# Kernel optimization log

Measured on AMD Instinct MI355X. Metric: run time of the kernel, lower is better.

Reference implementation:

```python
import jax, jax.numpy as jnp
import numpy as np
from jax import lax

# dims
B, N, K = 8, 1024, 32          # batch, nodes, kNN neighbors
D, H, DH = 256, 8, 32           # node feature width, heads, head dim
TDIM, NB, HID = 16, 32, 128     # time-embed dim, radial basis count, radial MLP hidden
NLAYERS = 3                     # hidden transformer layers
L = NLAYERS + 1                 # + output layer
NS = 128                        # scalar channels sliced into edge attrs
SHD = 9                         # spherical harmonics dim for lmax=2 (1+3+5)
RMAX = 2.0
EIN = NB + TDIM + 2 * NS        # edge-MLP input width


def _sph(u):
    # real spherical harmonics l=0,1,2 with 'component' normalization of unit vec u
    x, y, z = u[..., 0], u[..., 1], u[..., 2]
    l0 = jnp.ones_like(x)[..., None]
    l1 = np.sqrt(3.0) * u
    l2 = jnp.stack([
        np.sqrt(15.0) * x * y,
        np.sqrt(15.0) * y * z,
        0.5 * np.sqrt(5.0) * (3.0 * z * z - 1.0),
        np.sqrt(15.0) * x * z,
        0.5 * np.sqrt(15.0) * (x * x - y * y),
    ], -1)
    return jnp.concatenate([l0, l1, l2], -1)


def _rbf(r):
    # e3nn soft_one_hot_linspace(basis='gaussian', cutoff=False) * sqrt(NB) * 0.95
    centers = jnp.linspace(0.0, RMAX, NB)
    step = RMAX / (NB - 1)
    e = jnp.exp(-((r[..., None] - centers) / step) ** 2) / 1.12
    return e * (NB ** 0.5) * 0.95


def _sus(x):
    # e3nn smooth unit step: exp(-1/x) for x>0 else 0
    return jnp.where(x > 0, jnp.exp(-1.0 / jnp.where(x > 0, x, 1.0)), 0.0)


def setup_inputs() -> dict:
    key = jax.random.key(0)
    ks = jax.random.split(key, 12)
    g = lambda k, shape, fan: (jax.random.normal(k, shape, jnp.float32) / np.sqrt(fan))
    return {
        'x': jax.random.normal(ks[0], (B, N, 3), jnp.float32),
        'y': jax.random.normal(ks[1], (B, N, 3), jnp.float32),
        't': jax.random.uniform(ks[2], (B, TDIM), jnp.float32),
        'W_embed': g(ks[3], (3 + TDIM, D), 3 + TDIM),
        'Wk1': g(ks[4], (L, EIN, HID), EIN),
        'bk1': jnp.zeros((L, HID), jnp.float32),
        'Wk2': g(ks[5], (L, HID, H * DH), HID),
        'Wq': g(ks[6], (L, D, H * DH), D),
        'Wv': g(ks[7], (L, D + SHD, H * DH), D + SHD),
        'Wo': g(ks[8], (NLAYERS, H * DH, D), H * DH),
        'Wo_out': g(ks[9], (H * DH, 3), H * DH),
    }


def _forward(x, y, t, W_embed, Wk1, bk1, Wk2, Wq, Wv, Wo, Wo_out):
    def score(pos, feat, tt):
        # kNN graph: full pairwise distance + top_k (self included, as in source)
        d2 = jnp.sum((pos[:, None, :] - pos[None, :, :]) ** 2, -1)      # [N,N]
        src = lax.top_k(-d2, K)[1]                                       # [N,K], dst = row index
        vec = pos[:, None, :] - pos[src]                                 # pos[dst]-pos[src], [N,K,3]
        r = jnp.linalg.norm(vec, axis=-1)                                # [N,K]
        u = vec / jnp.maximum(r[..., None], 1e-9)
        sh = _sph(u)                                                     # [N,K,SHD]
        cut = 1.4 * _sus(10.0 * (1.0 - r / RMAX))                        # [N,K]
        rbf = _rbf(r) * cut[..., None]                                   # [N,K,NB]
        t_nodes = jnp.broadcast_to(tt, (N, TDIM))
        edge_base = jnp.concatenate([rbf, jnp.broadcast_to(tt, (N, K, TDIM))], -1)
        node = jnp.concatenate([feat, t_nodes], -1) @ W_embed            # [N,D]
        for l in range(L):
            # gather scalar node channels onto edges
            e = jnp.concatenate([edge_base, node[src][..., :NS],
                                 jnp.broadcast_to(node[:, None, :NS], (N, K, NS))], -1)  # [N,K,EIN]
            h = jax.nn.gelu(e @ Wk1[l] + bk1[l])                          # radial MLP
            kf = (h @ Wk2[l]).reshape(N, K, H, DH)
            q = (node @ Wq[l]).reshape(N, H, DH)
            logits = jnp.einsum('nhd,nkhd->nkh', q, kf) / np.sqrt(DH)
            # cutoff-weighted softmax over neighbors (e3nn Transformer style)
            w = cut[..., None] * jnp.exp(logits - logits.max(1, keepdims=True))
            alpha = w / (w.sum(1, keepdims=True) + 1e-9)                  # [N,K,H]
            v = (jnp.concatenate([node[src], sh], -1) @ Wv[l]).reshape(N, K, H, DH)
            agg = jnp.einsum('nkh,nkhd->nhd', alpha, v).reshape(N, H * DH)
            if l < NLAYERS:
                node = node + agg @ Wo[l]                                  # residual
                # scalar activation: gelu on 0e, tanh on 0o, identity on higher l
                node = jnp.concatenate([jax.nn.gelu(node[:, :64]),
                                        jnp.tanh(node[:, 64:NS]),
                                        node[:, NS:]], -1)
            else:
                node = agg @ Wo_out                                        # project to 1x1e
        return node  # [N,3]

    return jax.vmap(score)(x, y, t)


def reference(x, y, t, W_embed, Wk1, bk1, Wk2, Wq, Wv, Wo, Wo_out):
    return _forward(x, y, t, W_embed, Wk1, bk1, Wk2, Wq, Wv, Wo, Wo_out)
```

## Files before the change

### kernel.cpp

```cpp
#include <hip/hip_runtime.h>
#include <math.h>

#define Bb 8
#define Nn 1024
#define Kk 32
#define Dd 256
#define Hh 8
#define DHh 32
#define TDIMt 16
#define NBnb 32
#define HIDh 128
#define NSns 128
#define SHDs 9
#define EINe 304
#define NCOLS 1536

typedef __bf16 bf16_t;
typedef bf16_t bf16x8 __attribute__((ext_vector_type(8)));
typedef float floatx4 __attribute__((ext_vector_type(4)));

#define GLOAD_LDS16(gp, lp) __builtin_amdgcn_global_load_lds( \
    (const __attribute__((address_space(1))) void*)(gp),      \
    (__attribute__((address_space(3))) void*)(lp), 16, 0, 0)

__device__ __forceinline__ float gelu_fast(float x){
  float g = 1.5957691216057308f*(x + 0.044715f*x*x*x);
  return x*__builtin_amdgcn_rcpf(1.0f + __expf(-g));
}
__device__ __forceinline__ float tanh_fast(float x){
  return 1.0f - 2.0f*__builtin_amdgcn_rcpf(1.0f + __expf(2.0f*x));
}

__global__ __launch_bounds__(256) void setup_kernel(
    const float* __restrict__ x, const float* __restrict__ y, const float* __restrict__ t,
    const float* __restrict__ We, const float* __restrict__ Wk1, const float* __restrict__ bk1,
    const float* __restrict__ Wk2, const float* __restrict__ Wq, const float* __restrict__ Wv,
    const float* __restrict__ Wo,
    bf16_t* __restrict__ Wt, bf16_t* __restrict__ Wto, bf16_t* __restrict__ WrbfT,
    float* __restrict__ t_hd, int* __restrict__ src,
    float* __restrict__ node, bf16_t* __restrict__ node_bf){

  __shared__ float s_b[32];
  __shared__ unsigned long long s_knn[4][64];
  const int bid = blockIdx.x, tid = threadIdx.x;

  if (bid < 2048){
    int wave = tid >> 6, lane = tid & 63;
    int bn = bid*4 + wave;
    int b = bn >> 10, n = bn & (Nn-1);
    const float* xb = x + (size_t)b*Nn*3;
    float px = xb[n*3+0], py = xb[n*3+1], pz = xb[n*3+2];
    float d2v[16];
    #pragma unroll
    for (int i=0;i<16;i++){
      int j = i*64 + lane;
      float dx = px - xb[j*3+0];
      float dy = py - xb[j*3+1];
      float dz = pz - xb[j*3+2];
      d2v[i] = dx*dx + dy*dy + dz*dz;
    }

    unsigned lob = 0u, hib = 0x7149F2CAu;
    float T = 1.0f;
    int lc = 0;
    for (int it=0; it<24; ++it){
      lc = 0;
      #pragma unroll
      for (int i=0;i<16;i++) lc += (d2v[i] <= T) ? 1 : 0;
      int c = lc;
      #pragma unroll
      for (int off=32; off>=1; off>>=1) c += __shfl_xor(c, off);
      if (c >= 32 && c <= 64) break;
      if (c < 32) lob = __float_as_uint(T); else hib = __float_as_uint(T);
      float ratio = 44.0f * __builtin_amdgcn_rcpf((float)(c < 1 ? 1 : c));
      float Tn = T * __powf(ratio, 0.6666667f);
      unsigned tb = __float_as_uint(Tn);
      if (tb <= lob || tb >= hib) tb = lob + ((hib - lob) >> 1);
      T = __uint_as_float(tb);
    }

    int pre = lc;
    #pragma unroll
    for (int d=1; d<64; d<<=1){
      int o = __shfl_up(pre, d);
      if (lane >= d) pre += o;
    }
    int wo = pre - lc;

    unsigned long long* sl = s_knn[wave];
    sl[lane] = ~0ull;
    #pragma unroll
    for (int i=0;i<16;i++){
      if (d2v[i] <= T && wo < 64){
        sl[wo] = (((unsigned long long)__float_as_uint(d2v[i])) << 10)
                 | (unsigned)(i*64 + lane);
        wo++;
      }
    }
    __syncthreads();

    unsigned long long key = sl[lane];
    #pragma unroll
    for (int k2=2; k2<=64; k2<<=1){
      #pragma unroll
      for (int j2=k2>>1; j2>=1; j2>>=1){
        unsigned long long pv = __shfl_xor(key, j2);
        bool takeMin = (((lane & j2) == 0) == ((lane & k2) == 0));
        bool pLess = pv < key;
        key = (pLess == takeMin) ? pv : key;
      }
    }
    if (lane < 32) src[(size_t)bn*Kk + lane] = (int)(key & 1023u);
  } else if (bid < 6144){
    int i = bid-2048; int l = i>>10, yy = i&1023;
    int h = yy>>7, c = yy&127;
    if (tid < 32) s_b[tid] = Wk2[(size_t)l*HIDh*Dd + (size_t)c*Dd + h*DHh + tid];
    __syncthreads();
    const int rloc = tid>>3, dg = tid&7;
    const float b0 = s_b[dg*4+0], b1 = s_b[dg*4+1], b2 = s_b[dg*4+2], b3 = s_b[dg*4+3];
    #pragma unroll
    for (int p=0;p<8;p++){
      int ii = p*32 + rloc;
      const float4 v = *(const float4*)(Wq + (size_t)l*Dd*Dd + (size_t)ii*Dd + h*DHh + dg*4);
      float part = v.x*b0 + v.y*b1 + v.z*b2 + v.w*b3;
      part += __shfl_xor(part, 1);
      part += __shfl_xor(part, 2);
      part += __shfl_xor(part, 4);
      if (dg == 0) Wt[((size_t)l*NCOLS + 512 + yy)*Dd + ii] = (bf16_t)part;
    }
  } else if (bid < 8192){
    int i = bid-6144; int l = i>>9, c = i&511, k = tid;
    const float* wk1l = Wk1 + (size_t)l*EINe*HIDh;
    float v;
    if (c < 256)       v = Wv[(size_t)l*265*Dd + (size_t)k*Dd + c];
    else if (c < 384){ int c2 = c-256; v = (k < 128) ? wk1l[(48+k)*HIDh + c2] : 0.0f; }
    else             { int c2 = c-384; v = (k < 128) ? wk1l[(176+k)*HIDh + c2] : 0.0f; }
    Wt[((size_t)l*NCOLS + c)*Dd + k] = (bf16_t)v;
  } else if (bid < 8960){
    int i = bid-8192; int l = i>>8; int c = i&255; int k = tid;
    Wto[((size_t)l*Dd + c)*Dd + k] = (bf16_t)Wo[(size_t)l*Dd*Dd + (size_t)k*Dd + c];
  } else if (bid < 9024){
    int i = bid-8960; int l = i>>4, cg = i&15;
    int c = cg*8 + (tid>>5), k = tid&31;
    WrbfT[((size_t)l*HIDh + c)*NBnb + k] = (bf16_t)Wk1[(size_t)l*EINe*HIDh + (size_t)k*HIDh + c];
  } else if (bid < 9040){
    int i = bid-9024; int pair = i*2 + (tid>>7);
    int l = pair>>3, b = pair&7, c = tid&127;
    const float* wk1l = Wk1 + (size_t)l*EINe*HIDh;
    float a = bk1[l*HIDh + c];
    #pragma unroll
    for (int ii=0;ii<TDIMt;ii++) a += t[b*TDIMt+ii]*wk1l[(32+ii)*HIDh + c];
    t_hd[(l*Bb + b)*HIDh + c] = a;
  } else {
    int bn0 = (bid-9040)*4; int c = tid;
    float w0 = We[0*Dd+c], w1 = We[1*Dd+c], w2 = We[2*Dd+c];
    float wt[TDIMt];
    #pragma unroll
    for (int i=0;i<TDIMt;i++) wt[i] = We[(3+i)*Dd+c];
    #pragma unroll
    for (int u=0;u<4;u++){
      int bn = bn0 + u; int b = bn >> 10;
      float a = y[(size_t)bn*3+0]*w0 + y[(size_t)bn*3+1]*w1 + y[(size_t)bn*3+2]*w2;
      #pragma unroll
      for (int i=0;i<TDIMt;i++) a += t[b*TDIMt+i]*wt[i];
      node[(size_t)bn*Dd + c] = a;
      node_bf[(size_t)bn*Dd + c] = (bf16_t)a;
    }
  }
}

__global__ __launch_bounds__(256) void gemm_proj(const bf16_t* __restrict__ A,
    const bf16_t* __restrict__ Wt_all, float* __restrict__ vproj_f,
    bf16_t* __restrict__ hsrc_bf, float* __restrict__ hdst_f,
    bf16_t* __restrict__ qw_bf, const float* __restrict__ t_hd, int layer){

  __shared__ __align__(16) bf16_t s_A[2][8192];
  __shared__ __align__(16) bf16_t s_B[2][4096];

  const int tid = threadIdx.x;
  const int wave = tid>>6, lane = tid&63;
  const int row16 = lane&15, quad = lane>>4;
  const int bx = blockIdx.x;
  const int brow = ((bx & 7) << 3) + (bx >> 3);
  const int m0 = brow*128;
  const int m_base = m0 + wave*32;
  const int n_base = blockIdx.y*64;
  const bf16_t* Ab = A + (size_t)m0*Dd;
  const bf16_t* Bw = Wt_all + ((size_t)layer*NCOLS + n_base)*Dd;

  const int trow = tid>>3;
  const int tk   = ((tid&7) ^ (trow&7)) << 3;
  const int swz  = (row16&7) << 3;

  floatx4 acc[2][4];
  #pragma unroll
  for (int mi=0;mi<2;mi++)
    #pragma unroll
    for (int ni=0;ni<4;ni++){ floatx4 z = {0.f,0.f,0.f,0.f}; acc[mi][ni] = z; }

  {
    const bf16_t* ga = Ab + (size_t)trow*Dd + tk;
    #pragma unroll
    for (int i=0;i<4;i++) GLOAD_LDS16(ga + (size_t)i*32*Dd, &s_A[0][i*2048 + tid*8]);
    const bf16_t* gb = Bw + (size_t)trow*Dd + tk;
    #pragma unroll
    for (int j=0;j<2;j++) GLOAD_LDS16(gb + (size_t)j*32*Dd, &s_B[0][j*2048 + tid*8]);
  }
  __syncthreads();

  #pragma unroll
  for (int kt=0; kt<4; kt++){
    const int cur = kt&1, nxt = cur^1;
    if (kt < 3){
      const bf16_t* ga = Ab + (size_t)trow*Dd + (kt+1)*64 + tk;
      #pragma unroll
      for (int i=0;i<4;i++) GLOAD_LDS16(ga + (size_t)i*32*Dd, &s_A[nxt][i*2048 + tid*8]);
      const bf16_t* gb = Bw + (size_t)trow*Dd + (kt+1)*64 + tk;
      #pragma unroll
      for (int j=0;j<2;j++) GLOAD_LDS16(gb + (size_t)j*32*Dd, &s_B[nxt][j*2048 + tid*8]);
    }
    #pragma unroll
    for (int ksub=0; ksub<2; ksub++){
      const int ko = (ksub*32 + quad*8) ^ swz;
      bf16x8 a0 = *(const bf16x8*)&s_A[cur][(wave*32      + row16)*64 + ko];
      bf16x8 a1 = *(const bf16x8*)&s_A[cur][(wave*32 + 16 + row16)*64 + ko];
      #pragma unroll
      for (int ni=0;ni<4;ni++){
        bf16x8 b = *(const bf16x8*)&s_B[cur][(ni*16 + row16)*64 + ko];
        acc[0][ni] = __builtin_amdgcn_mfma_f32_16x16x32_bf16(a0, b, acc[0][ni], 0,0,0);
        acc[1][ni] = __builtin_amdgcn_mfma_f32_16x16x32_bf16(a1, b, acc[1][ni], 0,0,0);
      }
    }
    __syncthreads();
  }

  const int by = blockIdx.y;
  const int bb = m_base >> 10;
  #pragma unroll
  for (int mi=0;mi<2;mi++)
    #pragma unroll
    for (int ni=0;ni<4;ni++){
      int col = n_base + ni*16 + row16;
      #pragma unroll
      for (int r=0;r<4;r++){
        int row = m_base + mi*16 + quad*4 + r;
        float v = acc[mi][ni][r];
        if (by < 4)       vproj_f[(size_t)row*256 + col]        = v;
        else if (by < 6)  hsrc_bf[(size_t)row*128 + (col-256)]  = (bf16_t)v;
        else if (by < 8)  hdst_f[(size_t)row*128 + (col-384)]   = v + t_hd[(size_t)(layer*Bb + bb)*HIDh + (col-384)];
        else              qw_bf[(size_t)row*1024 + (col-512)]   = (bf16_t)v;
      }
    }
}

__global__ __launch_bounds__(256) void gemm_upd(
    const bf16_t* __restrict__ agg_bf, const bf16_t* __restrict__ Wto,
    const float* __restrict__ node_in, float* __restrict__ node_out,
    bf16_t* __restrict__ node_bf, int lu, int write_node){

  __shared__ __align__(16) bf16_t s_A[2][8192];
  __shared__ __align__(16) bf16_t s_B[2][4096];

  const int tid = threadIdx.x;
  const int wave = tid>>6, lane = tid&63;
  const int row16 = lane&15, quad = lane>>4;
  const int bx = blockIdx.x;
  const int brow = ((bx & 7) << 3) + (bx >> 3);
  const int m0 = brow*128;
  const int m_base = m0 + wave*32;
  const int n_base = blockIdx.y*64;
  const bf16_t* Ab = agg_bf + (size_t)m0*Dd;
  const bf16_t* Bw = Wto + (size_t)lu*Dd*Dd + (size_t)n_base*Dd;

  const int trow = tid>>3;
  const int tk   = ((tid&7) ^ (trow&7)) << 3;
  const int swz  = (row16&7) << 3;

  floatx4 acc[2][4];
  #pragma unroll
  for (int mi=0;mi<2;mi++)
    #pragma unroll
    for (int ni=0;ni<4;ni++){ floatx4 z = {0.f,0.f,0.f,0.f}; acc[mi][ni] = z; }

  {
    const bf16_t* ga = Ab + (size_t)trow*Dd + tk;
    #pragma unroll
    for (int i=0;i<4;i++) GLOAD_LDS16(ga + (size_t)i*32*Dd, &s_A[0][i*2048 + tid*8]);
    const bf16_t* gb = Bw + (size_t)trow*Dd + tk;
    #pragma unroll
    for (int j=0;j<2;j++) GLOAD_LDS16(gb + (size_t)j*32*Dd, &s_B[0][j*2048 + tid*8]);
  }
  __syncthreads();

  #pragma unroll
  for (int kt=0; kt<4; kt++){
    const int cur = kt&1, nxt = cur^1;
    if (kt < 3){
      const bf16_t* ga = Ab + (size_t)trow*Dd + (kt+1)*64 + tk;
      #pragma unroll
      for (int i=0;i<4;i++) GLOAD_LDS16(ga + (size_t)i*32*Dd, &s_A[nxt][i*2048 + tid*8]);
      const bf16_t* gb = Bw + (size_t)trow*Dd + (kt+1)*64 + tk;
      #pragma unroll
      for (int j=0;j<2;j++) GLOAD_LDS16(gb + (size_t)j*32*Dd, &s_B[nxt][j*2048 + tid*8]);
    }
    #pragma unroll
    for (int ksub=0; ksub<2; ksub++){
      const int ko = (ksub*32 + quad*8) ^ swz;
      bf16x8 a0 = *(const bf16x8*)&s_A[cur][(wave*32      + row16)*64 + ko];
      bf16x8 a1 = *(const bf16x8*)&s_A[cur][(wave*32 + 16 + row16)*64 + ko];
      #pragma unroll
      for (int ni=0;ni<4;ni++){
        bf16x8 b = *(const bf16x8*)&s_B[cur][(ni*16 + row16)*64 + ko];
        acc[0][ni] = __builtin_amdgcn_mfma_f32_16x16x32_bf16(a0, b, acc[0][ni], 0,0,0);
        acc[1][ni] = __builtin_amdgcn_mfma_f32_16x16x32_bf16(a1, b, acc[1][ni], 0,0,0);
      }
    }
    __syncthreads();
  }

  #pragma unroll
  for (int mi=0;mi<2;mi++)
    #pragma unroll
    for (int ni=0;ni<4;ni++){
      int col = n_base + ni*16 + row16;
      #pragma unroll
      for (int r=0;r<4;r++){
        int row = m_base + mi*16 + quad*4 + r;
        float v = acc[mi][ni][r] + node_in[(size_t)row*Dd + col];
        if (col < 64)       v = gelu_fast(v);
        else if (col < 128) v = tanh_fast(v);
        if (write_node) node_out[(size_t)row*Dd + col] = v;
        node_bf[(size_t)row*Dd + col] = (bf16_t)v;
      }
    }
}

__global__ __launch_bounds__(256) void attn_kernel(
    const float* __restrict__ x, const int* __restrict__ src,
    const float* __restrict__ vproj_f, const bf16_t* __restrict__ hsrc_bf,
    const float* __restrict__ hdst_f, const bf16_t* __restrict__ qw_bf,
    const bf16_t* __restrict__ WrbfT,
    const float* __restrict__ Wvg, const float* __restrict__ Woo,
    bf16_t* __restrict__ agg_bf, float* __restrict__ out, int layer){

  __shared__ __align__(16) char smem[11632];
  bf16_t* s_h     = (bf16_t*)(smem);
  float*  s_part  = (float*)(smem);
  float*  s_sh    = (float*)(smem + 8704);
  float*  s_cut   = (float*)(smem + 9984);
  int*    s_srcv  = (int*)  (smem + 10112);
  float*  s_logit = (float*)(smem + 10240);
  float*  s_poolsh= (float*)(smem + 11264);
  float*  s_red   = (float*)(smem + 11584);

  const int tid = threadIdx.x;
  const int bidx = blockIdx.x;
  const int bn  = ((bidx & 7) << 10) | (bidx >> 3);
  const int b   = bn >> 10;
  const int wave = tid>>6, lane = tid&63;
  const int row16 = lane&15, quad = lane>>4;

  bf16x8 qf[4];
  if (wave < 2){
    const bf16_t* qp = qw_bf + (size_t)bn*1024 + row16*HIDh + quad*8;
    #pragma unroll
    for (int ks=0; ks<4; ks++) qf[ks] = *(const bf16x8*)(qp + ks*32);
  }
  const float hdv0 = hdst_f[(size_t)bn*128 + wave*32 + row16];
  const float hdv1 = hdst_f[(size_t)bn*128 + wave*32 + 16 + row16];

  const float ax = x[(size_t)bn*3+0], ay = x[(size_t)bn*3+1], az = x[(size_t)bn*3+2];

  const int hr = tid>>4;
  const int hc = tid&15;
  const int sH0 = src[(size_t)bn*Kk + hr];
  const int sH1 = src[(size_t)bn*Kk + hr + 16];
  const int sE0 = src[(size_t)bn*Kk + row16];
  const int sE1 = src[(size_t)bn*Kk + row16 + 16];
  bf16x8 hsv0 = *(const bf16x8*)(hsrc_bf + ((size_t)b*Nn + sH0)*128 + hc*8);
  bf16x8 hsv1 = *(const bf16x8*)(hsrc_bf + ((size_t)b*Nn + sH1)*128 + hc*8);

  bf16x8 a0f, a1f;
  {
    const float* xj0 = x + ((size_t)b*Nn + sE0)*3;
    const float* xj1 = x + ((size_t)b*Nn + sE1)*3;
    float d0x = ax - xj0[0], d0y = ay - xj0[1], d0z = az - xj0[2];
    float d1x = ax - xj1[0], d1y = ay - xj1[1], d1z = az - xj1[2];
    float rr0 = sqrtf(d0x*d0x + d0y*d0y + d0z*d0z);
    float rr1 = sqrtf(d1x*d1x + d1y*d1y + d1z*d1z);
    float xx0 = 10.0f*(1.0f - rr0*0.5f);
    float xx1 = 10.0f*(1.0f - rr1*0.5f);
    float cu0 = (xx0 > 0.0f) ? 1.4f*__expf(-__builtin_amdgcn_rcpf(xx0)) : 0.0f;
    float cu1 = (xx1 > 0.0f) ? 1.4f*__expf(-__builtin_amdgcn_rcpf(xx1)) : 0.0f;
    float sc0 = 4.798224586623f*cu0;
    float sc1 = 4.798224586623f*cu1;
    float rs0 = fminf(rr0*15.5f, 33.0f);
    float rs1 = fminf(rr1*15.5f, 33.0f);
    float cbase = (float)(quad*8);
    float dd0 = rs0 - cbase, dd1 = rs1 - cbase;
    float e0 = __expf(-dd0*dd0)*sc0;
    float e1 = __expf(-dd1*dd1)*sc1;
    float g0 = __expf(2.0f*dd0 - 1.0f);
    float g1 = __expf(2.0f*dd1 - 1.0f);
    a0f[0] = (bf16_t)e0; a1f[0] = (bf16_t)e1;
    #pragma unroll
    for (int j=1;j<8;j++){
      e0 *= g0; e1 *= g1;
      a0f[j] = (bf16_t)e0; a1f[j] = (bf16_t)e1;
      g0 *= 0.13533528323661270f; g1 *= 0.13533528323661270f;
    }
  }

  if (tid < 32){
    int k = tid;
    int j = src[(size_t)bn*Kk + k];
    s_srcv[k] = j;
    const float* xj = x + ((size_t)b*Nn + j)*3;
    float dx = ax - xj[0], dy = ay - xj[1], dz = az - xj[2];
    float rr = sqrtf(dx*dx + dy*dy + dz*dz);
    float xx = 10.0f*(1.0f - rr*0.5f);
    s_cut[k] = (xx > 0.0f) ? 1.4f*__expf(-__builtin_amdgcn_rcpf(xx)) : 0.0f;
  } else if (tid < 64){
    int k = tid - 32;
    int j = src[(size_t)bn*Kk + k];
    const float* xj = x + ((size_t)b*Nn + j)*3;
    float dx = ax - xj[0], dy = ay - xj[1], dz = az - xj[2];
    float rr = sqrtf(dx*dx + dy*dy + dz*dz);
    float inv = __builtin_amdgcn_rcpf(fmaxf(rr, 1e-9f));
    float ux = dx*inv, uy = dy*inv, uz = dz*inv;
    float* sh = s_sh + k*10;
    sh[0] = 1.0f;
    sh[1] = 1.7320508075688772f*ux;
    sh[2] = 1.7320508075688772f*uy;
    sh[3] = 1.7320508075688772f*uz;
    sh[4] = 3.872983346207417f*ux*uy;
    sh[5] = 3.872983346207417f*uy*uz;
    sh[6] = 1.118033988749895f*(3.0f*uz*uz - 1.0f);
    sh[7] = 3.872983346207417f*ux*uz;
    sh[8] = 1.9364916731037085f*(ux*ux - uy*uy);
  }

  floatx4 acc[2][2];
  {
    #pragma unroll
    for (int mi=0;mi<2;mi++)
      #pragma unroll
      for (int ni=0;ni<2;ni++){ floatx4 z = {0.f,0.f,0.f,0.f}; acc[mi][ni] = z; }
    const bf16_t* bp = WrbfT + ((size_t)layer*HIDh + wave*32 + row16)*NBnb + quad*8;
    bf16x8 b0 = *(const bf16x8*)(bp);
    bf16x8 b1 = *(const bf16x8*)(bp + 16*NBnb);
    acc[0][0] = __builtin_amdgcn_mfma_f32_16x16x32_bf16(a0f, b0, acc[0][0], 0,0,0);
    acc[0][1] = __builtin_amdgcn_mfma_f32_16x16x32_bf16(a0f, b1, acc[0][1], 0,0,0);
    acc[1][0] = __builtin_amdgcn_mfma_f32_16x16x32_bf16(a1f, b0, acc[1][0], 0,0,0);
    acc[1][1] = __builtin_amdgcn_mfma_f32_16x16x32_bf16(a1f, b1, acc[1][1], 0,0,0);
  }
  *(bf16x8*)(s_h + hr*136 + hc*8)      = hsv0;
  *(bf16x8*)(s_h + (hr+16)*136 + hc*8) = hsv1;
  __syncthreads();

  #pragma unroll
  for (int ni=0;ni<2;ni++){
    int c = wave*32 + ni*16 + row16;
    float hdv = ni ? hdv1 : hdv0;
    #pragma unroll
    for (int mi=0;mi<2;mi++){
      #pragma unroll
      for (int r=0;r<4;r++){
        int e = mi*16 + quad*4 + r;
        float hs = (float)s_h[e*136 + c];
        s_h[e*136 + c] = (bf16_t)gelu_fast(acc[mi][ni][r] + hdv + hs);
      }
    }
  }
  __syncthreads();

  if (wave < 2){
    floatx4 la = {0.f,0.f,0.f,0.f};
    #pragma unroll
    for (int ks=0; ks<4; ks++){
      bf16x8 a = *(const bf16x8*)(s_h + (wave*16 + row16)*136 + ks*32 + quad*8);
      la = __builtin_amdgcn_mfma_f32_16x16x32_bf16(a, qf[ks], la, 0,0,0);
    }
    if (row16 < Hh){
      #pragma unroll
      for (int r=0;r<4;r++)
        s_logit[(wave*16 + quad*4 + r)*8 + row16] = la[r]*0.17677669529663687f;
    }
  }
  __syncthreads();

  {
    const int k = tid & 31;
    const int h = tid >> 5;
    float lv = s_logit[k*8 + h];
    float m = lv;
    #pragma unroll
    for (int off=16; off>=1; off>>=1) m = fmaxf(m, __shfl_xor(m, off));
    float w = s_cut[k]*__expf(lv - m);
    float ss = w;
    #pragma unroll
    for (int off=16; off>=1; off>>=1) ss += __shfl_xor(ss, off);
    float alpha = w*__builtin_amdgcn_rcpf(ss + 1e-9f);
    s_logit[k*8 + h] = alpha;
  }
  __syncthreads();

  {
    const float* rowp[8];
    #pragma unroll
    for (int i=0;i<8;i++){
      int row = __builtin_amdgcn_readfirstlane(s_srcv[wave*8 + i]);
      rowp[i] = vproj_f + ((size_t)b*Nn + row)*256;
    }
    const int al_base = wave*64 + (lane>>3);
    float4 accv = {0.f,0.f,0.f,0.f};
    #pragma unroll
    for (int i=0;i<8;i++){
      const float4 v = *(const float4*)(rowp[i] + (lane<<2));
      float al = s_logit[al_base + i*8];
      accv.x += al*v.x; accv.y += al*v.y; accv.z += al*v.z; accv.w += al*v.w;
    }

    if (wave >= 2){
      const int tt = tid - 128;
      const int h2 = tt >> 4, sg = tt & 15;
      if (sg < SHDs){
        float a = 0.0f;
        #pragma unroll
        for (int k2=0;k2<Kk;k2++)
          a += s_logit[k2*8 + h2] * s_sh[k2*10 + sg];
        s_poolsh[h2*10 + sg] = a;
      }
    }

    *(float4*)(s_part + wave*256 + (lane<<2)) = accv;
  }
  __syncthreads();

  {
    const int h = tid >> 5;
    float a_main = s_part[tid] + s_part[256+tid] + s_part[512+tid] + s_part[768+tid];

    const float* wvsh = Wvg + (size_t)layer*265*Dd + 256*Dd;
    #pragma unroll
    for (int sg=0; sg<SHDs; sg++) a_main += s_poolsh[h*10 + sg]*wvsh[sg*Dd + tid];

    if (layer < 3){
      agg_bf[(size_t)bn*Dd + tid] = (bf16_t)a_main;
    } else {
      float p0 = a_main*Woo[tid*3+0];
      float p1 = a_main*Woo[tid*3+1];
      float p2 = a_main*Woo[tid*3+2];
      #pragma unroll
      for (int off=32; off>=1; off>>=1){
        p0 += __shfl_xor(p0, off);
        p1 += __shfl_xor(p1, off);
        p2 += __shfl_xor(p2, off);
      }
      if (lane == 0){ s_red[wave*3+0]=p0; s_red[wave*3+1]=p1; s_red[wave*3+2]=p2; }
      __syncthreads();
      if (tid < 3)
        out[(size_t)bn*3 + tid] = s_red[0*3+tid]+s_red[1*3+tid]+s_red[2*3+tid]+s_red[3*3+tid];
    }
  }
}

extern "C" void kernel_launch(void* const* d_in, const int* in_sizes, int n_in,
                              void* d_out, int out_size, void* d_ws, size_t ws_size,
                              hipStream_t stream){
  const float* x   = (const float*)d_in[0];
  const float* y   = (const float*)d_in[1];
  const float* t   = (const float*)d_in[2];
  const float* We  = (const float*)d_in[3];
  const float* Wk1 = (const float*)d_in[4];
  const float* bk1 = (const float*)d_in[5];
  const float* Wk2 = (const float*)d_in[6];
  const float* Wq  = (const float*)d_in[7];
  const float* Wv  = (const float*)d_in[8];
  const float* Wo  = (const float*)d_in[9];
  const float* Woo = (const float*)d_in[10];
  float* out = (float*)d_out;

  char* ws = (char*)d_ws;
  size_t off = 0;
  auto take = [&](size_t bytes)->char*{ char* p = ws + off; off = (off + bytes + 255) & ~(size_t)255; return p; };

  int*    src      = (int*)   take((size_t)Bb*Nn*Kk*4);
  float*  nodeA    = (float*) take((size_t)Bb*Nn*Dd*4);
  float*  nodeB    = (float*) take((size_t)Bb*Nn*Dd*4);
  bf16_t* node_bf  = (bf16_t*)take((size_t)Bb*Nn*Dd*2);
  bf16_t* agg_bf   = (bf16_t*)take((size_t)Bb*Nn*Dd*2);
  float*  vproj_f  = (float*) take((size_t)Bb*Nn*256*4);
  bf16_t* hsrc_bf  = (bf16_t*)take((size_t)Bb*Nn*128*2);
  float*  hdst_f   = (float*) take((size_t)Bb*Nn*128*4);
  bf16_t* qw_bf    = (bf16_t*)take(((size_t)Bb*Nn*1024 + 2048)*2);
  bf16_t* Wt       = (bf16_t*)take((size_t)4*NCOLS*Dd*2);
  bf16_t* Wto      = (bf16_t*)take((size_t)3*Dd*Dd*2);
  bf16_t* WrbfT    = (bf16_t*)take((size_t)4*HIDh*NBnb*2);
  float*  t_hd     = (float*) take((size_t)4*Bb*HIDh*4);

  setup_kernel<<<dim3(11088), 256, 0, stream>>>(x, y, t, We, Wk1, bk1, Wk2, Wq, Wv, Wo,
                                                Wt, Wto, WrbfT, t_hd, src, nodeA, node_bf);

  gemm_proj<<<dim3(64,24), 256, 0, stream>>>(node_bf, Wt, vproj_f, hsrc_bf, hdst_f, qw_bf, t_hd, 0);
  attn_kernel<<<dim3(Bb*Nn), 256, 0, stream>>>(x, src, vproj_f, hsrc_bf, hdst_f, qw_bf,
                                               WrbfT, Wv, Woo, agg_bf, out, 0);
  const float* nin[3]  = {nodeA, nodeB, nodeA};
  float*       nout[3] = {nodeB, nodeA, nodeB};
  for (int l=1; l<4; l++){
    gemm_upd<<<dim3(64,4), 256, 0, stream>>>(agg_bf, Wto, nin[l-1], nout[l-1], node_bf,
                                             l-1, (l < 3) ? 1 : 0);
    gemm_proj<<<dim3(64,24), 256, 0, stream>>>(node_bf, Wt, vproj_f, hsrc_bf, hdst_f, qw_bf, t_hd, l);
    attn_kernel<<<dim3(Bb*Nn), 256, 0, stream>>>(x, src, vproj_f, hsrc_bf, hdst_f, qw_bf,
                                                 WrbfT, Wv, Woo, agg_bf, out, l);
  }
}
```

Baseline: 404.9 us.

## Process two destination nodes per attention block to use all waves

The attention kernel now handles two nodes per 256-thread block, with two waves per node, and the grid is halved. Before, only two of the four waves did the logit MFMA and the other waves idled or did side work. Now every wave does MFMA work, and the Wv spherical-harmonic weights and RBF weight loads are shared across two nodes. Shared memory roughly doubles, and each wave handles 16 neighbor rows of value gathers, so per-wave latency and register pressure rise and occupancy may drop.

```diff
diff --git a/kernel.cpp b/kernel.cpp
--- a/kernel.cpp
+++ b/kernel.cpp
@@ -343,42 +343,46 @@
     const float* __restrict__ Wvg, const float* __restrict__ Woo,
     bf16_t* __restrict__ agg_bf, float* __restrict__ out, int layer){
 
-  __shared__ __align__(16) char smem[11632];
+  __shared__ __align__(16) char smem[23296];
   bf16_t* s_h     = (bf16_t*)(smem);
   float*  s_part  = (float*)(smem);
-  float*  s_sh    = (float*)(smem + 8704);
-  float*  s_cut   = (float*)(smem + 9984);
-  int*    s_srcv  = (int*)  (smem + 10112);
-  float*  s_logit = (float*)(smem + 10240);
-  float*  s_poolsh= (float*)(smem + 11264);
-  float*  s_red   = (float*)(smem + 11584);
-
-  const int tid = threadIdx.x;
+  float*  s_sh    = (float*)(smem + 17408);
+  float*  s_cut   = (float*)(smem + 19968);
+  int*    s_srcv  = (int*)  (smem + 20224);
+  float*  s_logit = (float*)(smem + 20480);
+  float*  s_pool  = (float*)(smem + 22528);
+  float*  s_red   = (float*)(smem + 23168);
+
+  const int tid  = threadIdx.x;
   const int bidx = blockIdx.x;
-  const int bn  = ((bidx & 7) << 10) | (bidx >> 3);
-  const int b   = bn >> 10;
+  const int b    = bidx & 7;
+  const int bn0  = (b << 10) | ((bidx >> 3) << 1);
   const int wave = tid>>6, lane = tid&63;
+  const int side = wave>>1, wv = wave&1;
   const int row16 = lane&15, quad = lane>>4;
+  const int bns = bn0 + side;
 
   bf16x8 qf[4];
-  if (wave < 2){
-    const bf16_t* qp = qw_bf + (size_t)bn*1024 + row16*HIDh + quad*8;
-    #pragma unroll
-    for (int ks=0; ks<4; ks++) qf[ks] = *(const bf16x8*)(qp + ks*32);
-  }
-  const float hdv0 = hdst_f[(size_t)bn*128 + wave*32 + row16];
-  const float hdv1 = hdst_f[(size_t)bn*128 + wave*32 + 16 + row16];
-
-  const float ax = x[(size_t)bn*3+0], ay = x[(size_t)bn*3+1], az = x[(size_t)bn*3+2];
-
-  const int hr = tid>>4;
-  const int hc = tid&15;
-  const int sH0 = src[(size_t)bn*Kk + hr];
-  const int sH1 = src[(size_t)bn*Kk + hr + 16];
-  const int sE0 = src[(size_t)bn*Kk + row16];
-  const int sE1 = src[(size_t)bn*Kk + row16 + 16];
-  bf16x8 hsv0 = *(const bf16x8*)(hsrc_bf + ((size_t)b*Nn + sH0)*128 + hc*8);
-  bf16x8 hsv1 = *(const bf16x8*)(hsrc_bf + ((size_t)b*Nn + sH1)*128 + hc*8);
+  { const bf16_t* qp = qw_bf + (size_t)bns*1024 + row16*HIDh + quad*8;
+    #pragma unroll
+    for (int ks=0; ks<4; ks++) qf[ks] = *(const bf16x8*)(qp + ks*32); }
+  float hdv[4];
+  #pragma unroll
+  for (int ni=0; ni<4; ni++) hdv[ni] = hdst_f[(size_t)bns*128 + wv*64 + ni*16 + row16];
+
+  const float ax = x[(size_t)bns*3+0], ay = x[(size_t)bns*3+1], az = x[(size_t)bns*3+2];
+
+  const int sE0 = src[(size_t)bns*Kk + row16];
+  const int sE1 = src[(size_t)bns*Kk + row16 + 16];
+
+  const int t2 = tid & 127;
+  const int e0 = t2>>3, cg = t2&7;
+  const int sG0 = src[(size_t)bns*Kk + e0];
+  const int sG1 = src[(size_t)bns*Kk + e0 + 16];
+  bf16x8 hsv00 = *(const bf16x8*)(hsrc_bf + ((size_t)b*Nn + sG0)*128 + cg*8);
+  bf16x8 hsv01 = *(const bf16x8*)(hsrc_bf + ((size_t)b*Nn + sG0)*128 + cg*8 + 64);
+  bf16x8 hsv10 = *(const bf16x8*)(hsrc_bf + ((size_t)b*Nn + sG1)*128 + cg*8);
+  bf16x8 hsv11 = *(const bf16x8*)(hsrc_bf + ((size_t)b*Nn + sG1)*128 + cg*8 + 64);
 
   bf16x8 a0f, a1f;
   {
@@ -398,93 +402,96 @@
     float rs1 = fminf(rr1*15.5f, 33.0f);
     float cbase = (float)(quad*8);
     float dd0 = rs0 - cbase, dd1 = rs1 - cbase;
-    float e0 = __expf(-dd0*dd0)*sc0;
-    float e1 = __expf(-dd1*dd1)*sc1;
+    float e0v = __expf(-dd0*dd0)*sc0;
+    float e1v = __expf(-dd1*dd1)*sc1;
     float g0 = __expf(2.0f*dd0 - 1.0f);
     float g1 = __expf(2.0f*dd1 - 1.0f);
-    a0f[0] = (bf16_t)e0; a1f[0] = (bf16_t)e1;
+    a0f[0] = (bf16_t)e0v; a1f[0] = (bf16_t)e1v;
     #pragma unroll
     for (int j=1;j<8;j++){
-      e0 *= g0; e1 *= g1;
-      a0f[j] = (bf16_t)e0; a1f[j] = (bf16_t)e1;
+      e0v *= g0; e1v *= g1;
+      a0f[j] = (bf16_t)e0v; a1f[j] = (bf16_t)e1v;
       g0 *= 0.13533528323661270f; g1 *= 0.13533528323661270f;
     }
   }
 
-  if (tid < 32){
-    int k = tid;
-    int j = src[(size_t)bn*Kk + k];
-    s_srcv[k] = j;
+  if (tid < 128){
+    const int hs = (tid>>6)&1;
+    const int k = tid & 31;
+    const int hn = bn0 + hs;
+    const int j = src[(size_t)hn*Kk + k];
+    const float hx = x[(size_t)hn*3+0], hy = x[(size_t)hn*3+1], hz = x[(size_t)hn*3+2];
     const float* xj = x + ((size_t)b*Nn + j)*3;
-    float dx = ax - xj[0], dy = ay - xj[1], dz = az - xj[2];
+    float dx = hx - xj[0], dy = hy - xj[1], dz = hz - xj[2];
     float rr = sqrtf(dx*dx + dy*dy + dz*dz);
-    float xx = 10.0f*(1.0f - rr*0.5f);
-    s_cut[k] = (xx > 0.0f) ? 1.4f*__expf(-__builtin_amdgcn_rcpf(xx)) : 0.0f;
-  } else if (tid < 64){
-    int k = tid - 32;
-    int j = src[(size_t)bn*Kk + k];
-    const float* xj = x + ((size_t)b*Nn + j)*3;
-    float dx = ax - xj[0], dy = ay - xj[1], dz = az - xj[2];
-    float rr = sqrtf(dx*dx + dy*dy + dz*dz);
-    float inv = __builtin_amdgcn_rcpf(fmaxf(rr, 1e-9f));
-    float ux = dx*inv, uy = dy*inv, uz = dz*inv;
-    float* sh = s_sh + k*10;
-    sh[0] = 1.0f;
-    sh[1] = 1.7320508075688772f*ux;
-    sh[2] = 1.7320508075688772f*uy;
-    sh[3] = 1.7320508075688772f*uz;
-    sh[4] = 3.872983346207417f*ux*uy;
-    sh[5] = 3.872983346207417f*uy*uz;
-    sh[6] = 1.118033988749895f*(3.0f*uz*uz - 1.0f);
-    sh[7] = 3.872983346207417f*ux*uz;
-    sh[8] = 1.9364916731037085f*(ux*ux - uy*uy);
-  }
-
-  floatx4 acc[2][2];
+    if ((tid & 32) == 0){
+      s_srcv[hs*32 + k] = j;
+      float xx = 10.0f*(1.0f - rr*0.5f);
+      s_cut[hs*32 + k] = (xx > 0.0f) ? 1.4f*__expf(-__builtin_amdgcn_rcpf(xx)) : 0.0f;
+    } else {
+      float inv = __builtin_amdgcn_rcpf(fmaxf(rr, 1e-9f));
+      float ux = dx*inv, uy = dy*inv, uz = dz*inv;
+      float* sh = s_sh + hs*320 + k*10;
+      sh[0] = 1.0f;
+      sh[1] = 1.7320508075688772f*ux;
+      sh[2] = 1.7320508075688772f*uy;
+      sh[3] = 1.7320508075688772f*uz;
+      sh[4] = 3.872983346207417f*ux*uy;
+      sh[5] = 3.872983346207417f*uy*uz;
+      sh[6] = 1.118033988749895f*(3.0f*uz*uz - 1.0f);
+      sh[7] = 3.872983346207417f*ux*uz;
+      sh[8] = 1.9364916731037085f*(ux*ux - uy*uy);
+    }
+  }
+
+  floatx4 acc[2][4];
   {
     #pragma unroll
     for (int mi=0;mi<2;mi++)
       #pragma unroll
-      for (int ni=0;ni<2;ni++){ floatx4 z = {0.f,0.f,0.f,0.f}; acc[mi][ni] = z; }
-    const bf16_t* bp = WrbfT + ((size_t)layer*HIDh + wave*32 + row16)*NBnb + quad*8;
-    bf16x8 b0 = *(const bf16x8*)(bp);
-    bf16x8 b1 = *(const bf16x8*)(bp + 16*NBnb);
-    acc[0][0] = __builtin_amdgcn_mfma_f32_16x16x32_bf16(a0f, b0, acc[0][0], 0,0,0);
-    acc[0][1] = __builtin_amdgcn_mfma_f32_16x16x32_bf16(a0f, b1, acc[0][1], 0,0,0);
-    acc[1][0] = __builtin_amdgcn_mfma_f32_16x16x32_bf16(a1f, b0, acc[1][0], 0,0,0);
-    acc[1][1] = __builtin_amdgcn_mfma_f32_16x16x32_bf16(a1f, b1, acc[1][1], 0,0,0);
-  }
-  *(bf16x8*)(s_h + hr*136 + hc*8)      = hsv0;
-  *(bf16x8*)(s_h + (hr+16)*136 + hc*8) = hsv1;
+      for (int ni=0;ni<4;ni++){ floatx4 z = {0.f,0.f,0.f,0.f}; acc[mi][ni] = z; }
+    const bf16_t* bp = WrbfT + ((size_t)layer*HIDh + wv*64 + row16)*NBnb + quad*8;
+    #pragma unroll
+    for (int j=0;j<4;j++){
+      bf16x8 bbf = *(const bf16x8*)(bp + (size_t)j*16*NBnb);
+      acc[0][j] = __builtin_amdgcn_mfma_f32_16x16x32_bf16(a0f, bbf, acc[0][j], 0,0,0);
+      acc[1][j] = __builtin_amdgcn_mfma_f32_16x16x32_bf16(a1f, bbf, acc[1][j], 0,0,0);
+    }
+  }
+
+  bf16_t* shs = s_h + side*4352;
+  *(bf16x8*)(shs + e0*136 + cg*8)            = hsv00;
+  *(bf16x8*)(shs + e0*136 + cg*8 + 64)       = hsv01;
+  *(bf16x8*)(shs + (e0+16)*136 + cg*8)       = hsv10;
+  *(bf16x8*)(shs + (e0+16)*136 + cg*8 + 64)  = hsv11;
   __syncthreads();
 
   #pragma unroll
-  for (int ni=0;ni<2;ni++){
-    int c = wave*32 + ni*16 + row16;
-    float hdv = ni ? hdv1 : hdv0;
+  for (int ni=0;ni<4;ni++){
+    int c = wv*64 + ni*16 + row16;
     #pragma unroll
     for (int mi=0;mi<2;mi++){
       #pragma unroll
       for (int r=0;r<4;r++){
         int e = mi*16 + quad*4 + r;
-        float hs = (float)s_h[e*136 + c];
-        s_h[e*136 + c] = (bf16_t)gelu_fast(acc[mi][ni][r] + hdv + hs);
+        float hs = (float)shs[e*136 + c];
+        shs[e*136 + c] = (bf16_t)gelu_fast(acc[mi][ni][r] + hdv[ni] + hs);
       }
     }
   }
   __syncthreads();
 
-  if (wave < 2){
+  {
     floatx4 la = {0.f,0.f,0.f,0.f};
     #pragma unroll
     for (int ks=0; ks<4; ks++){
-      bf16x8 a = *(const bf16x8*)(s_h + (wave*16 + row16)*136 + ks*32 + quad*8);
+      bf16x8 a = *(const bf16x8*)(shs + (wv*16 + row16)*136 + ks*32 + quad*8);
       la = __builtin_amdgcn_mfma_f32_16x16x32_bf16(a, qf[ks], la, 0,0,0);
     }
     if (row16 < Hh){
       #pragma unroll
       for (int r=0;r<4;r++)
-        s_logit[(wave*16 + quad*4 + r)*8 + row16] = la[r]*0.17677669529663687f;
+        s_logit[side*256 + (wv*16 + quad*4 + r)*8 + row16] = la[r]*0.17677669529663687f;
     }
   }
   __syncthreads();
@@ -492,75 +499,94 @@
   {
     const int k = tid & 31;
     const int h = tid >> 5;
-    float lv = s_logit[k*8 + h];
-    float m = lv;
-    #pragma unroll
-    for (int off=16; off>=1; off>>=1) m = fmaxf(m, __shfl_xor(m, off));
-    float w = s_cut[k]*__expf(lv - m);
-    float ss = w;
-    #pragma unroll
-    for (int off=16; off>=1; off>>=1) ss += __shfl_xor(ss, off);
-    float alpha = w*__builtin_amdgcn_rcpf(ss + 1e-9f);
-    s_logit[k*8 + h] = alpha;
+    #pragma unroll
+    for (int sn=0; sn<2; sn++){
+      float lv = s_logit[sn*256 + k*8 + h];
+      float m = lv;
+      #pragma unroll
+      for (int off=16; off>=1; off>>=1) m = fmaxf(m, __shfl_xor(m, off));
+      float w = s_cut[sn*32 + k]*__expf(lv - m);
+      float ss = w;
+      #pragma unroll
+      for (int off=16; off>=1; off>>=1) ss += __shfl_xor(ss, off);
+      s_logit[sn*256 + k*8 + h] = w*__builtin_amdgcn_rcpf(ss + 1e-9f);
+    }
   }
   __syncthreads();
 
   {
-    const float* rowp[8];
-    #pragma unroll
-    for (int i=0;i<8;i++){
-      int row = __builtin_amdgcn_readfirstlane(s_srcv[wave*8 + i]);
+    const int pn = tid>>7, t3 = tid&127, h2 = t3>>4, sg = t3&15;
+    if (sg < SHDs){
+      float a = 0.0f;
+      #pragma unroll
+      for (int k2=0;k2<Kk;k2++)
+        a += s_logit[pn*256 + k2*8 + h2] * s_sh[pn*320 + k2*10 + sg];
+      s_pool[pn*80 + h2*10 + sg] = a;
+    }
+  }
+
+  {
+    const float* rowp[16];
+    #pragma unroll
+    for (int i=0;i<16;i++){
+      int row = __builtin_amdgcn_readfirstlane(s_srcv[side*32 + wv*16 + i]);
       rowp[i] = vproj_f + ((size_t)b*Nn + row)*256;
     }
-    const int al_base = wave*64 + (lane>>3);
+    const int albase = side*256 + wv*128 + (lane>>3);
     float4 accv = {0.f,0.f,0.f,0.f};
     #pragma unroll
-    for (int i=0;i<8;i++){
+    for (int i=0;i<16;i++){
       const float4 v = *(const float4*)(rowp[i] + (lane<<2));
-      float al = s_logit[al_base + i*8];
+      float al = s_logit[albase + i*8];
       accv.x += al*v.x; accv.y += al*v.y; accv.z += al*v.z; accv.w += al*v.w;
     }
-
-    if (wave >= 2){
-      const int tt = tid - 128;
-      const int h2 = tt >> 4, sg = tt & 15;
-      if (sg < SHDs){
-        float a = 0.0f;
+    *(float4*)(s_part + (side*2 + wv)*256 + (lane<<2)) = accv;
+  }
+  __syncthreads();
+
+  {
+    const int h = tid >> 5;
+    const float* wvsh = Wvg + (size_t)layer*265*Dd + 256*Dd;
+    float wv9[SHDs];
+    #pragma unroll
+    for (int sg=0; sg<SHDs; sg++) wv9[sg] = wvsh[sg*Dd + tid];
+
+    float w0=0.f, w1=0.f, w2=0.f;
+    if (layer >= 3){ w0 = Woo[tid*3+0]; w1 = Woo[tid*3+1]; w2 = Woo[tid*3+2]; }
+
+    #pragma unroll
+    for (int sn=0; sn<2; sn++){
+      float a_main = s_part[sn*512 + tid] + s_part[sn*512 + 256 + tid];
+      #pragma unroll
+      for (int sg=0; sg<SHDs; sg++) a_main += s_pool[sn*80 + h*10 + sg]*wv9[sg];
+
+      if (layer < 3){
+        agg_bf[(size_t)(bn0+sn)*Dd + tid] = (bf16_t)a_main;
+      } else {
+        float p0 = a_main*w0;
+        float p1 = a_main*w1;
+        float p2 = a_main*w2;
         #pragma unroll
-        for (int k2=0;k2<Kk;k2++)
-          a += s_logit[k2*8 + h2] * s_sh[k2*10 + sg];
-        s_poolsh[h2*10 + sg] = a;
-      }
-    }
-
-    *(float4*)(s_part + wave*256 + (lane<<2)) = accv;
-  }
-  __syncthreads();
-
-  {
-    const int h = tid >> 5;
-    float a_main = s_part[tid] + s_part[256+tid] + s_part[512+tid] + s_part[768+tid];
-
-    const float* wvsh = Wvg + (size_t)layer*265*Dd + 256*Dd;
-    #pragma unroll
-    for (int sg=0; sg<SHDs; sg++) a_main += s_poolsh[h*10 + sg]*wvsh[sg*Dd + tid];
-
-    if (layer < 3){
-      agg_bf[(size_t)bn*Dd + tid] = (bf16_t)a_main;
-    } else {
-      float p0 = a_main*Woo[tid*3+0];
-      float p1 = a_main*Woo[tid*3+1];
-      float p2 = a_main*Woo[tid*3+2];
-      #pragma unroll
-      for (int off=32; off>=1; off>>=1){
-        p0 += __shfl_xor(p0, off);
-        p1 += __shfl_xor(p1, off);
-        p2 += __shfl_xor(p2, off);
-      }
-      if (lane == 0){ s_red[wave*3+0]=p0; s_red[wave*3+1]=p1; s_red[wave*3+2]=p2; }
+        for (int off=32; off>=1; off>>=1){
+          p0 += __shfl_xor(p0, off);
+          p1 += __shfl_xor(p1, off);
+          p2 += __shfl_xor(p2, off);
+        }
+        if (lane == 0){
+          s_red[sn*12 + wave*3+0] = p0;
+          s_red[sn*12 + wave*3+1] = p1;
+          s_red[sn*12 + wave*3+2] = p2;
+        }
+      }
+    }
+    if (layer >= 3){
       __syncthreads();
-      if (tid < 3)
-        out[(size_t)bn*3 + tid] = s_red[0*3+tid]+s_red[1*3+tid]+s_red[2*3+tid]+s_red[3*3+tid];
+      if (tid < 8){
+        int sn = tid>>2, j = tid&3;
+        if (j < 3)
+          out[(size_t)(bn0+sn)*3 + j] = s_red[sn*12 + j] + s_red[sn*12 + 3 + j]
+                                      + s_red[sn*12 + 6 + j] + s_red[sn*12 + 9 + j];
+      }
     }
   }
 }
@@ -603,15 +629,15 @@
                                                 Wt, Wto, WrbfT, t_hd, src, nodeA, node_bf);
 
   gemm_proj<<<dim3(64,24), 256, 0, stream>>>(node_bf, Wt, vproj_f, hsrc_bf, hdst_f, qw_bf, t_hd, 0);
-  attn_kernel<<<dim3(Bb*Nn), 256, 0, stream>>>(x, src, vproj_f, hsrc_bf, hdst_f, qw_bf,
-                                               WrbfT, Wv, Woo, agg_bf, out, 0);
+  attn_kernel<<<dim3(Bb*Nn/2), 256, 0, stream>>>(x, src, vproj_f, hsrc_bf, hdst_f, qw_bf,
+                                                 WrbfT, Wv, Woo, agg_bf, out, 0);
   const float* nin[3]  = {nodeA, nodeB, nodeA};
   float*       nout[3] = {nodeB, nodeA, nodeB};
   for (int l=1; l<4; l++){
     gemm_upd<<<dim3(64,4), 256, 0, stream>>>(agg_bf, Wto, nin[l-1], nout[l-1], node_bf,
                                              l-1, (l < 3) ? 1 : 0);
     gemm_proj<<<dim3(64,24), 256, 0, stream>>>(node_bf, Wt, vproj_f, hsrc_bf, hdst_f, qw_bf, t_hd, l);
-    attn_kernel<<<dim3(Bb*Nn), 256, 0, stream>>>(x, src, vproj_f, hsrc_bf, hdst_f, qw_bf,
-                                                 WrbfT, Wv, Woo, agg_bf, out, l);
+    attn_kernel<<<dim3(Bb*Nn/2), 256, 0, stream>>>(x, src, vproj_f, hsrc_bf, hdst_f, qw_bf,
+                                                   WrbfT, Wv, Woo, agg_bf, out, l);
   }
 }
```

Result: faster. 391.4 us (-3.4%).
